# Kernel optimization log

Measured on AMD Instinct MI355X. Metric: run time of the kernel, lower is better.

Reference implementation:

```python
import jax, jax.numpy as jnp
import numpy as np

D_MODEL = 2048
N_HEADS = 16
N_KV = 4
HEAD_DIM = 128
SUB = 64
WINDOW = 512
THETA = 10000.0
NEG = jnp.float32(-1e30)


def _rope_tables(seq_len):
    inv_freq = 1.0 / (THETA ** (jnp.arange(0, HEAD_DIM, 2, dtype=jnp.float32) / HEAD_DIM))
    freqs = jnp.arange(seq_len, dtype=jnp.float32)[:, None] * inv_freq[None, :]  # [S, hd/2]
    emb = jnp.concatenate([freqs, freqs], axis=-1)  # [S, hd]
    return jnp.cos(emb), jnp.sin(emb)


def _rotate_half(x):
    x1, x2 = x[..., : HEAD_DIM // 2], x[..., HEAD_DIM // 2 :]
    return jnp.concatenate([-x2, x1], axis=-1)


def _apply_rope(t, cos, sin):
    # t: [B, H, S, hd]; cos/sin: [S, hd]
    c = cos[None, None]
    s = sin[None, None]
    return t * c + _rotate_half(t) * s


def setup_inputs() -> dict:
    key = jax.random.key(0)
    ks = jax.random.split(key, 6)
    B, S = 1, 2048
    std = 0.02
    return {
        "x": jax.random.normal(ks[0], (B, S, D_MODEL), dtype=jnp.float32),
        "Wq": jax.random.normal(ks[1], (D_MODEL, N_HEADS * HEAD_DIM), dtype=jnp.float32) * std,
        "Wk": jax.random.normal(ks[2], (D_MODEL, N_KV * HEAD_DIM), dtype=jnp.float32) * std,
        "Wv": jax.random.normal(ks[3], (D_MODEL, N_KV * HEAD_DIM), dtype=jnp.float32) * std,
        "Wo": jax.random.normal(ks[4], (N_HEADS * HEAD_DIM, D_MODEL), dtype=jnp.float32) * std,
        "lam": jnp.full((N_HEADS,), 0.1, dtype=jnp.float32),
    }


def reference(x, Wq, Wk, Wv, Wo, lam):
    B, S, _ = x.shape
    n_rep = N_HEADS // N_KV

    q = (x @ Wq).reshape(B, S, N_HEADS, HEAD_DIM).transpose(0, 2, 1, 3)  # [B,H,S,hd]
    k = (x @ Wk).reshape(B, S, N_KV, HEAD_DIM).transpose(0, 2, 1, 3)    # [B,KH,S,hd]
    v = (x @ Wv).reshape(B, S, N_KV, HEAD_DIM).transpose(0, 2, 1, 3)

    cos, sin = _rope_tables(S)
    q = _apply_rope(q, cos, sin)
    k = _apply_rope(k, cos, sin)

    # GQA repeat: each kv head replicated n_rep times consecutively
    k = jnp.repeat(k, n_rep, axis=1)  # [B,H,S,hd]
    v = jnp.repeat(v, n_rep, axis=1)

    q1, q2 = q[..., :SUB], q[..., SUB:]
    k1, k2 = k[..., :SUB], k[..., SUB:]
    scale = 1.0 / jnp.sqrt(jnp.float32(SUB))

    s1 = jnp.einsum("bhqd,bhkd->bhqk", q1, k1) * scale
    s2 = jnp.einsum("bhqd,bhkd->bhqk", q2, k2) * scale

    i = jnp.arange(S)[:, None]
    j = jnp.arange(S)[None, :]
    allowed = (j <= i) & (j >= i - WINDOW + 1)  # causal + sliding window
    s1 = jnp.where(allowed[None, None], s1, NEG)
    s2 = jnp.where(allowed[None, None], s2, NEG)

    a1 = jax.nn.softmax(s1.astype(jnp.float32), axis=-1).astype(x.dtype)
    a2 = jax.nn.softmax(s2.astype(jnp.float32), axis=-1).astype(x.dtype)

    diff = jax.nn.relu(a1 - lam[None, :, None, None] * a2)
    diff = diff / (jnp.sum(diff, axis=-1, keepdims=True) + 1e-6)

    out = jnp.einsum("bhqk,bhkd->bhqd", diff, v)  # [B,H,S,hd]
    out = out.transpose(0, 2, 1, 3).reshape(B, S, N_HEADS * HEAD_DIM)
    return out @ Wo
```

## Files before the change

### kernel.cpp

```cpp
#include <hip/hip_runtime.h>
#include <hip/hip_bf16.h>
#include <stdint.h>

typedef __attribute__((ext_vector_type(8))) short short8;
typedef __attribute__((ext_vector_type(4))) float f32x4;
using bf16 = __hip_bfloat16;

#define MFMA16(a, b, c) __builtin_amdgcn_mfma_f32_16x16x32_bf16((a), (b), (c), 0, 0, 0)

#define GLOAD_LDS16(g, l) __builtin_amdgcn_global_load_lds( \
    (const __attribute__((address_space(1))) void*)(g),     \
    (__attribute__((address_space(3))) void*)(l), 16, 0, 0)

__device__ __forceinline__ unsigned packbf2(float lo, float hi) {
  unsigned r;
  asm("v_cvt_pk_bf16_f32 %0, %1, %2" : "=v"(r) : "v"(lo), "v"(hi));
  return r;
}
__device__ __forceinline__ float ex2(float x) {
  float r;
  asm("v_exp_f32 %0, %1" : "=v"(r) : "v"(x));
  return r;
}
__device__ __forceinline__ f32x4 vmax4(f32x4 a, f32x4 b) {
  f32x4 r;
  r[0] = fmaxf(a[0], b[0]); r[1] = fmaxf(a[1], b[1]);
  r[2] = fmaxf(a[2], b[2]); r[3] = fmaxf(a[3], b[3]);
  return r;
}

template <bool EDGE>
__device__ __forceinline__ void p1_update(const f32x4* sv, float& m, float& l,
                                          int kb0, int myq, int lhi) {
  f32x4 t4 = vmax4(vmax4(sv[0], sv[1]), vmax4(sv[2], sv[3]));
  float tm = fmaxf(fmaxf(t4[0], t4[1]), fmaxf(t4[2], t4[3]));
  float nm = fmaxf(m, tm);
  float sc = ex2(m - nm);
  float sum = 0.f;
#pragma unroll
  for (int nt = 0; nt < 4; ++nt) {
    float part = 0.f;
#pragma unroll
    for (int r = 0; r < 4; ++r) {
      float e = ex2(sv[nt][r] - nm);
      if (EDGE) {
        int key = kb0 + nt * 16 + lhi * 4 + r;
        bool ok = (key <= myq) && (key > myq - 512);
        e = ok ? e : 0.f;
      }
      part += e;
    }
    sum += part;
  }
  l = l * sc + sum;
  m = nm;
}

template <bool EDGE>
__device__ __forceinline__ float p2_probs(const f32x4* s1v, const f32x4* s2v,
                                          float m1, float m2, float c2,
                                          int kb0, int myq, int lhi, int l15,
                                          unsigned* pw) {
  float d0 = 0.f, d1 = 0.f;
#pragma unroll
  for (int nt = 0; nt < 4; ++nt) {
    float pr[4];
#pragma unroll
    for (int r = 0; r < 4; ++r) {
      float e1 = ex2(s1v[nt][r] - m1);
      float e2 = ex2(s2v[nt][r] - m2);
      float p = fmaf(-c2, e2, e1);
      p = fmaxf(p, 0.f);
      if (EDGE) {
        int key = kb0 + nt * 16 + lhi * 4 + r;
        bool ok = (key <= myq) && (key > myq - 512);
        p = ok ? p : 0.f;
      }
      pr[r] = p;
      if (r & 1) d1 += p; else d0 += p;
    }
    int pi = l15 * 36 + 8 * nt + 2 * lhi;
    pw[pi]     = packbf2(pr[0], pr[1]);
    pw[pi + 1] = packbf2(pr[2], pr[3]);
  }
  return d0 + d1;
}

__global__ __launch_bounds__(256) void prep_all(const float* __restrict__ x,
                                                const float* __restrict__ Wq,
                                                const float* __restrict__ Wk,
                                                const float* __restrict__ Wv,
                                                const float* __restrict__ Wo,
                                                bf16* __restrict__ xb,
                                                bf16* __restrict__ WqkvFT,
                                                bf16* __restrict__ WoFT)
{
  const int bx = blockIdx.x;
  const int tid = threadIdx.x;
  if (bx >= 80) {
    size_t i = ((size_t)(bx - 80) * 32 + blockIdx.y) * 2048 + tid * 8;
    const float* f = x + i;
    float4 a = *(const float4*)f;
    float4 b = *(const float4*)(f + 4);
    union { bf16 h[8]; short8 s; } u;
    u.h[0] = __float2bfloat16(a.x); u.h[1] = __float2bfloat16(a.y);
    u.h[2] = __float2bfloat16(a.z); u.h[3] = __float2bfloat16(a.w);
    u.h[4] = __float2bfloat16(b.x); u.h[5] = __float2bfloat16(b.y);
    u.h[6] = __float2bfloat16(b.z); u.h[7] = __float2bfloat16(b.w);
    *(short8*)(xb + i) = u.s;
    return;
  }
  const float* W;
  bf16* Wt;
  int N, n0;
  if (bx < 32)      { W = Wq; Wt = WqkvFT; N = 2048; n0 = bx * 64; }
  else if (bx < 40) { W = Wk; Wt = WqkvFT; N = 512;  n0 = 2048 + (bx - 32) * 64; }
  else if (bx < 48) { W = Wv; Wt = WqkvFT; N = 512;  n0 = 2560 + (bx - 40) * 64; }
  else              { W = Wo; Wt = WoFT;   N = 2048; n0 = (bx - 48) * 64; }
  const int nloc0 = (N == 512) ? (n0 - ((n0 >= 2560) ? 2560 : 2048)) : ((bx < 32 || bx >= 48) ? (n0 & 2047) : 0);
  const int k0 = blockIdx.y * 64;

  __shared__ bf16 t[64][72];
#pragma unroll
  for (int pass = 0; pass < 4; ++pass) {
    int r = pass * 16 + (tid >> 4);
    int c = (tid & 15) * 4;
    float4 v = *(const float4*)(W + (size_t)(k0 + r) * N + nloc0 + c);
    t[c + 0][r] = __float2bfloat16(v.x);
    t[c + 1][r] = __float2bfloat16(v.y);
    t[c + 2][r] = __float2bfloat16(v.z);
    t[c + 3][r] = __float2bfloat16(v.w);
  }
  __syncthreads();
#pragma unroll
  for (int pass = 0; pass < 2; ++pass) {
    int n = pass * 32 + (tid >> 3);
    int k8 = (tid & 7) * 8;
    int frag = ((n0 + n) >> 4) * 64 + ((k0 + k8) >> 5);
    int ln = (n & 15) + 16 * ((k8 >> 3) & 3);
    *(short8*)(Wt + (size_t)frag * 512 + ln * 8) = *(const short8*)(&t[n][k8]);
  }
}

template <int EPI>
__global__ __launch_bounds__(256) void gemm_ft(const bf16* __restrict__ A,
                                               const bf16* __restrict__ Bft,
                                               void* __restrict__ C,
                                               bf16* __restrict__ VTp,
                                               int M, int N, int K)
{
  __shared__ __align__(16) bf16 As[4][128 * 32];

  const int tid  = threadIdx.x;
  const int lane = tid & 63;
  const int w    = tid >> 6;
  const int wmg  = (w >> 1) * 4;
  const int wng  = (w & 1) * 4;
  const int l15  = lane & 15;
  const int lhi  = lane >> 4;

  const int nbx = gridDim.x;
  const int lb  = blockIdx.y * nbx + blockIdx.x;
  const int nwg = nbx * gridDim.y;
  const int lsw = (lb & 7) * (nwg >> 3) + (lb >> 3);
  const int bm0 = (lsw / nbx) * 128;
  const int bn0 = (lsw % nbx) * 128;

  const int srow = lane >> 2;
  const int scol = ((lane & 3) ^ ((lane >> 3) & 3)) * 8;
  const int loff = l15 * 4 + (lhi ^ ((l15 >> 1) & 3));

  const int nkc = K >> 5;
  const bf16* bbase[4];
#pragma unroll
  for (int nt = 0; nt < 4; ++nt)
    bbase[nt] = Bft + ((size_t)((bn0 >> 4) + wng + nt) * nkc) * 512 + lane * 8;

  f32x4 acc[4][4];
  const f32x4 zero4 = {0.f, 0.f, 0.f, 0.f};
#pragma unroll
  for (int i = 0; i < 4; ++i)
#pragma unroll
    for (int j = 0; j < 4; ++j) acc[i][j] = zero4;

  short8 br0[4], br1[4], br2[4], br3[4];

#define GSTAGE_A(buf, kk)                                                          \
  { _Pragma("unroll")                                                              \
    for (int p = 0; p < 2; ++p) {                                                  \
      int s   = (p * 4 + w) * 64 + lane;                                           \
      int row = (p * 4 + w) * 16 + srow;                                           \
      GLOAD_LDS16(A + (size_t)(bm0 + row) * K + (kk) + scol, &As[buf][s * 8]);     \
    } }

#define BLOAD(breg, kc)                                                            \
  { _Pragma("unroll")                                                              \
    for (int nt = 0; nt < 4; ++nt) {                                               \
      asm volatile("global_load_dwordx4 %0, %1, off"                               \
                   : "=v"(breg[nt])                                                \
                   : "v"(bbase[nt] + (size_t)(kc) * 512)                           \
                   : "memory");                                                    \
    } }

#define KSTEP(aslot, breg, wcn, ...)                                               \
  {                                                                                \
    asm volatile("s_waitcnt vmcnt(" #wcn ")" ::: "memory");                        \
    __builtin_amdgcn_s_barrier();                                                  \
    __builtin_amdgcn_sched_barrier(0);                                             \
    __VA_ARGS__                                                                    \
    short8 a_[4];                                                                  \
    _Pragma("unroll")                                                              \
    for (int mt = 0; mt < 4; ++mt)                                                 \
      a_[mt] = *(const short8*)(&As[aslot][((wmg + mt) * 64 + loff) * 8]);         \
    _Pragma("unroll")                                                              \
    for (int mt = 0; mt < 4; ++mt)                                                 \
      _Pragma("unroll")                                                            \
      for (int nt = 0; nt < 4; ++nt)                                               \
        acc[mt][nt] = MFMA16(a_[mt], breg[nt], acc[mt][nt]);                       \
  }

  GSTAGE_A(0, 0);  BLOAD(br0, 0);
  GSTAGE_A(1, 32); BLOAD(br1, 1);
  GSTAGE_A(2, 64); BLOAD(br2, 2);

  for (int t = 0; t < nkc - 4; t += 4) {
    KSTEP(0, br0, 12, GSTAGE_A(3, (t + 3) * 32); BLOAD(br3, t + 3);)
    KSTEP(1, br1, 12, GSTAGE_A(0, (t + 4) * 32); BLOAD(br0, t + 4);)
    KSTEP(2, br2, 12, GSTAGE_A(1, (t + 5) * 32); BLOAD(br1, t + 5);)
    KSTEP(3, br3, 12, GSTAGE_A(2, (t + 6) * 32); BLOAD(br2, t + 6);)
  }
  KSTEP(0, br0, 12, GSTAGE_A(3, (nkc - 1) * 32); BLOAD(br3, nkc - 1);)
  KSTEP(1, br1, 12, )
  KSTEP(2, br2, 6, )
  KSTEP(3, br3, 0, )
#undef GSTAGE_A
#undef BLOAD
#undef KSTEP

  if (EPI == 1) {
#pragma unroll
    for (int mt = 0; mt < 4; ++mt) {
      int row0 = bm0 + (wmg + mt) * 16 + lhi * 4;
#pragma unroll
      for (int nt = 0; nt < 4; ++nt) {
        int col = bn0 + (wng + nt) * 16 + l15;
#pragma unroll
        for (int r = 0; r < 4; ++r)
          ((float*)C)[(size_t)(row0 + r) * N + col] = acc[mt][nt][r];
      }
    }
    return;
  }

  __syncthreads();
  if (bn0 < 2560) {
    float* Lf = (float*)&As[0][0];
    const float scale = (bn0 < 2048) ? 0.180336880111120f : 1.0f;
#pragma unroll
    for (int c = 0; c < 2; ++c) {
      if ((w >> 1) == c) {
#pragma unroll
        for (int mt = 0; mt < 4; ++mt)
#pragma unroll
          for (int nt = 0; nt < 4; ++nt) {
            int col = (wng + nt) * 16 + l15;
#pragma unroll
            for (int r = 0; r < 4; ++r)
              Lf[(mt * 16 + lhi * 4 + r) * 128 + col] = acc[mt][nt][r];
          }
      }
      __syncthreads();
      {
        int rloc = tid >> 2;
        int dg = (tid & 3) * 16;
        int s = bm0 + c * 64 + rloc;
        bf16* orow = (bf16*)C + (size_t)s * N + bn0;
        union { bf16 h[16]; short8 v[2]; } o1, o2;
#pragma unroll
        for (int e = 0; e < 16; ++e) {
          int d = dg + e;
          float inv = __expf(-(float)d * (9.210340371976184f / 64.0f));
          float ang = (float)s * inv;
          float cs = __cosf(ang), sn = __sinf(ang);
          float x1 = Lf[rloc * 128 + d];
          float x2 = Lf[rloc * 128 + d + 64];
          o1.h[e] = __float2bfloat16((x1 * cs - x2 * sn) * scale);
          o2.h[e] = __float2bfloat16((x2 * cs + x1 * sn) * scale);
        }
        *(short8*)(orow + dg)      = o1.v[0];
        *(short8*)(orow + dg + 8)  = o1.v[1];
        *(short8*)(orow + dg + 64) = o2.v[0];
        *(short8*)(orow + dg + 72) = o2.v[1];
      }
      __syncthreads();
    }
  } else {
    bf16* Lb = &As[0][0];
#pragma unroll
    for (int cc = 0; cc < 2; ++cc) {
      if ((w & 1) == cc) {
#pragma unroll
        for (int mt = 0; mt < 4; ++mt)
#pragma unroll
          for (int nt = 0; nt < 4; ++nt) {
            int colloc = nt * 16 + l15;
#pragma unroll
            for (int r = 0; r < 4; ++r) {
              int key = (wmg + mt) * 16 + lhi * 4 + r;
              Lb[colloc * 136 + key] = __float2bfloat16(acc[mt][nt][r]);
            }
          }
      }
      __syncthreads();
      {
        int dl = tid >> 2;
        int kq = (tid & 3) * 32;
        int dim = (bn0 - 2560) + cc * 64 + dl;
        bf16* vrow = VTp + (size_t)dim * 2048 + bm0 + kq;
#pragma unroll
        for (int j = 0; j < 4; ++j)
          *(short8*)(vrow + j * 8) = *(const short8*)(&Lb[dl * 136 + kq + j * 8]);
      }
      __syncthreads();
    }
  }
}

__global__ __launch_bounds__(256) void diff_attn(const bf16* __restrict__ QKV,
                                                 const bf16* __restrict__ VT,
                                                 const float* __restrict__ lam,
                                                 bf16* __restrict__ O)
{
  __shared__ __align__(16) bf16 Kb[2][64 * 128];
  __shared__ __align__(16) bf16 Vb[2][128 * 64];
  __shared__ __align__(16) bf16 Pw[4][16 * 72];

  const int lb  = blockIdx.y * 32 + blockIdx.x;
  const int lsw = (lb & 7) * 64 + (lb >> 3);
  const int qb  = lsw & 31;
  const int h   = lsw >> 5;

  const int kvh  = h >> 2;
  const int tid  = threadIdx.x;
  const int lane = tid & 63;
  const int w    = tid >> 6;
  const int l15  = lane & 15;
  const int lhi  = lane >> 4;
  const int qg   = qb * 64 + w * 16;
  const int myq  = qg + l15;
  const float lamv = lam[h];

  const bf16* Kg = QKV + 2048 + (size_t)kvh * 128;
  const bf16* Vg = VT + (size_t)kvh * 128 * 2048;

  short8 qf[4];
  {
    const bf16* qrow = QKV + (size_t)myq * 3072 + h * 128;
#pragma unroll
    for (int c = 0; c < 4; ++c)
      qf[c] = *(const short8*)(qrow + c * 32 + lhi * 8);
  }

  const int t0 = (qb >= 8) ? (qb - 8) : 0;

#define STAGE_K(buf, kbase)                                                     \
  {                                                                             \
    _Pragma("unroll")                                                           \
    for (int p = 0; p < 4; ++p) {                                               \
      int c = p * 256 + tid;                                                    \
      int r = c >> 4, q = c & 15;                                               \
      GLOAD_LDS16(Kg + (size_t)((kbase) + r) * 3072 + ((q ^ (r & 7)) * 8),      \
                  &Kb[buf][c * 8]);                                             \
    }                                                                           \
  }
#define STAGE_V(buf, kbase)                                                     \
  {                                                                             \
    _Pragma("unroll")                                                           \
    for (int p = 0; p < 4; ++p) {                                               \
      int c = p * 256 + tid;                                                    \
      int d = c >> 3, q = c & 7;                                                \
      GLOAD_LDS16(Vg + (size_t)d * 2048 + (kbase) + ((q ^ (d & 7)) * 8),        \
                  &Vb[buf][c * 8]);                                             \
    }                                                                           \
  }
#define KFRAG(buf, nt, qc) \
  (*(const short8*)(&Kb[buf][(((nt) * 16 + l15) * 16 + ((qc) ^ (((nt) * 16 + l15) & 7))) * 8]))
#define VFRAG(buf, n, qc) \
  (*(const short8*)(&Vb[buf][(((n) * 16 + l15) * 8 + ((qc) ^ (((n) * 16 + l15) & 7))) * 8]))
#define QK_TILE(cur)                                            \
  _Pragma("unroll")                                             \
  for (int nt = 0; nt < 4; ++nt) {                              \
    f32x4 s1 = zero4, s2 = zero4;                               \
    s1 = MFMA16(KFRAG(cur, nt, lhi),      qf[0], s1);           \
    s1 = MFMA16(KFRAG(cur, nt, 4 + lhi),  qf[1], s1);           \
    s2 = MFMA16(KFRAG(cur, nt, 8 + lhi),  qf[2], s2);           \
    s2 = MFMA16(KFRAG(cur, nt, 12 + lhi), qf[3], s2);           \
    s1v[nt] = s1; s2v[nt] = s2;                                 \
  }

  const f32x4 zero4 = {0.f, 0.f, 0.f, 0.f};

  float m1 = -1e30f, l1 = 0.f, m2 = -1e30f, l2 = 0.f;
  STAGE_K(0, t0 * 64);
  asm volatile("s_waitcnt vmcnt(0)" ::: "memory");
  __builtin_amdgcn_s_barrier();
  {
    int cur = 0;
    for (int t = t0; t <= qb; ++t, cur ^= 1) {
      if (t < qb) {
        STAGE_K(cur ^ 1, (t + 1) * 64);
        asm volatile("s_waitcnt vmcnt(4)" ::: "memory");
      } else {
        asm volatile("s_waitcnt vmcnt(0)" ::: "memory");
      }
      __builtin_amdgcn_s_barrier();
      __builtin_amdgcn_sched_barrier(0);
      const int kb0 = t * 64;
      f32x4 s1v[4], s2v[4];
      QK_TILE(cur);
      const bool edge = (t == qb) || (qb >= 8 && t == t0);
      if (edge) {
        p1_update<true>(s1v, m1, l1, kb0, myq, lhi);
        p1_update<true>(s2v, m2, l2, kb0, myq, lhi);
      } else {
        p1_update<false>(s1v, m1, l1, kb0, myq, lhi);
        p1_update<false>(s2v, m2, l2, kb0, myq, lhi);
      }
      __builtin_amdgcn_s_barrier();
    }
  }

#pragma unroll
  for (int mk = 16; mk <= 32; mk <<= 1) {
    float pm = __shfl_xor(m1, mk, 64), pl = __shfl_xor(l1, mk, 64);
    float M = fmaxf(m1, pm);
    l1 = l1 * ex2(m1 - M) + pl * ex2(pm - M);
    m1 = M;
    pm = __shfl_xor(m2, mk, 64); pl = __shfl_xor(l2, mk, 64);
    M = fmaxf(m2, pm);
    l2 = l2 * ex2(m2 - M) + pl * ex2(pm - M);
    m2 = M;
  }
  const float c2 = lamv * l1 / l2;

  f32x4 accv[8];
#pragma unroll
  for (int n = 0; n < 8; ++n) accv[n] = zero4;
  float dln = 0.f;

  STAGE_K(0, t0 * 64);
  STAGE_V(0, t0 * 64);
  asm volatile("s_waitcnt vmcnt(0)" ::: "memory");
  __builtin_amdgcn_s_barrier();
  {
    int cur = 0;
    for (int t = t0; t <= qb; ++t, cur ^= 1) {
      if (t < qb) {
        STAGE_K(cur ^ 1, (t + 1) * 64);
        STAGE_V(cur ^ 1, (t + 1) * 64);
        asm volatile("s_waitcnt vmcnt(8)" ::: "memory");
      } else {
        asm volatile("s_waitcnt vmcnt(0)" ::: "memory");
      }
      __builtin_amdgcn_s_barrier();
      __builtin_amdgcn_sched_barrier(0);
      const int kb0 = t * 64;
      unsigned* pw = (unsigned*)&Pw[w][0];
      f32x4 s1v[4], s2v[4];
      QK_TILE(cur);
      const bool edge = (t == qb) || (qb >= 8 && t == t0);
      if (edge) dln += p2_probs<true>(s1v, s2v, m1, m2, c2, kb0, myq, lhi, l15, pw);
      else      dln += p2_probs<false>(s1v, s2v, m1, m2, c2, kb0, myq, lhi, l15, pw);
#pragma unroll
      for (int kc = 0; kc < 2; ++kc) {
        short8 pa = *(const short8*)(&Pw[w][l15 * 72 + kc * 32 + lhi * 8]);
#pragma unroll
        for (int n = 0; n < 8; ++n)
          accv[n] = MFMA16(pa, VFRAG(cur, n, kc * 4 + lhi), accv[n]);
      }
      __builtin_amdgcn_s_barrier();
    }
  }

  dln += __shfl_xor(dln, 16, 64);
  dln += __shfl_xor(dln, 32, 64);

#pragma unroll
  for (int r = 0; r < 4; ++r) {
    int srcq = lhi * 4 + r;
    int src = (lane & 48) | srcq;
    float dq = __shfl(dln, src, 64);
    float lq = __shfl(l1, src, 64);
    float rinv = 1.f / (dq + lq * 1e-6f);
    int qo = qg + srcq;
#pragma unroll
    for (int n = 0; n < 8; ++n) {
      O[(size_t)qo * 2048 + h * 128 + n * 16 + l15] =
          __float2bfloat16(accv[n][r] * rinv);
    }
  }
#undef STAGE_K
#undef STAGE_V
#undef KFRAG
#undef VFRAG
#undef QK_TILE
}

extern "C" void kernel_launch(void* const* d_in, const int* in_sizes, int n_in,
                              void* d_out, int out_size, void* d_ws, size_t ws_size,
                              hipStream_t stream)
{
  const float* x   = (const float*)d_in[0];
  const float* Wq  = (const float*)d_in[1];
  const float* Wk  = (const float*)d_in[2];
  const float* Wv  = (const float*)d_in[3];
  const float* Wo  = (const float*)d_in[4];
  const float* lam = (const float*)d_in[5];

  char* ws = (char*)d_ws;
  bf16* xb     = (bf16*)(ws);
  bf16* WqkvFT = (bf16*)(ws + 8ull  * (1u << 20));
  bf16* WoFT   = (bf16*)(ws + 20ull * (1u << 20));
  bf16* QKV    = (bf16*)(ws + 28ull * (1u << 20));
  bf16* ATT    = (bf16*)(ws + 40ull * (1u << 20));
  bf16* VT     = (bf16*)(ws + 48ull * (1u << 20));

  prep_all<<<dim3(144, 32), 256, 0, stream>>>(x, Wq, Wk, Wv, Wo, xb, WqkvFT, WoFT);
  gemm_ft<0><<<dim3(24, 16), 256, 0, stream>>>(xb, WqkvFT, QKV, VT, 2048, 3072, 2048);
  diff_attn<<<dim3(32, 16), 256, 0, stream>>>(QKV, VT, lam, ATT);
  gemm_ft<1><<<dim3(16, 16), 256, 0, stream>>>(ATT, WoFT, d_out, nullptr, 2048, 2048, 2048);
}
```

Before: 110.9 us.

## Split QKV GEMM into dedicated 128x256-tile 512-thread kernel with direct V-transpose stores

The QKV projection gets its own kernel with 8 waves and a 128x256 output tile. This halves the grid to 192 workgroups and lets each A tile in LDS be reused across twice as many output columns. The V epilogue now packs accumulators and writes the transposed layout straight to global memory, with no LDS staging or extra barriers. The output-projection GEMM is split into its own plain fp32-store kernel. Risks are fewer workgroups than CUs (192 on a 256-CU part), higher register pressure, and scattered 8-byte stores for the V transpose.

```diff
diff --git a/kernel.cpp b/kernel.cpp
--- a/kernel.cpp
+++ b/kernel.cpp
@@ -142,11 +142,162 @@
   }
 }
 
-template <int EPI>
-__global__ __launch_bounds__(256) void gemm_ft(const bf16* __restrict__ A,
+__global__ __launch_bounds__(512) void gemm_qkv(const bf16* __restrict__ A,
+                                                const bf16* __restrict__ Bft,
+                                                bf16* __restrict__ QKV,
+                                                bf16* __restrict__ VTp,
+                                                int M, int N, int K)
+{
+  __shared__ __align__(16) char smem[65536];
+  bf16* As = (bf16*)smem;
+
+  const int tid  = threadIdx.x;
+  const int lane = tid & 63;
+  const int w    = tid >> 6;
+  const int wmg  = (w >> 2) * 4;
+  const int wng  = (w & 3) * 4;
+  const int l15  = lane & 15;
+  const int lhi  = lane >> 4;
+
+  const int nbx = gridDim.x;
+  const int lb  = blockIdx.y * nbx + blockIdx.x;
+  const int nwg = nbx * gridDim.y;
+  const int lsw = (lb & 7) * (nwg >> 3) + (lb >> 3);
+  const int bm0 = (lsw / nbx) * 128;
+  const int bn0 = (lsw % nbx) * 256;
+
+  const int srow = tid >> 2;
+  const int scol = ((tid & 3) ^ ((tid >> 3) & 3)) * 8;
+  const int loff = l15 * 4 + (lhi ^ ((l15 >> 1) & 3));
+
+  const int nkc = K >> 5;
+  const bf16* bbase[4];
+#pragma unroll
+  for (int nt = 0; nt < 4; ++nt)
+    bbase[nt] = Bft + ((size_t)((bn0 >> 4) + wng + nt) * nkc) * 512 + lane * 8;
+
+  f32x4 acc[4][4];
+  const f32x4 zero4 = {0.f, 0.f, 0.f, 0.f};
+#pragma unroll
+  for (int i = 0; i < 4; ++i)
+#pragma unroll
+    for (int j = 0; j < 4; ++j) acc[i][j] = zero4;
+
+  short8 br0[4], br1[4], br2[4], br3[4];
+
+#define GSTAGE_A(buf, kk)                                                           \
+  { GLOAD_LDS16(A + (size_t)(bm0 + srow) * K + (kk) + scol,                         \
+                As + (buf) * 4096 + tid * 8); }
+
+#define BLOAD(breg, kc)                                                             \
+  { _Pragma("unroll")                                                               \
+    for (int nt = 0; nt < 4; ++nt) {                                                \
+      asm volatile("global_load_dwordx4 %0, %1, off"                                \
+                   : "=v"(breg[nt])                                                 \
+                   : "v"(bbase[nt] + (size_t)(kc) * 512)                            \
+                   : "memory");                                                     \
+    } }
+
+#define KSTEP(aslot, breg, wcn, ...)                                                \
+  {                                                                                 \
+    asm volatile("s_waitcnt vmcnt(" #wcn ")" ::: "memory");                         \
+    __builtin_amdgcn_s_barrier();                                                   \
+    __builtin_amdgcn_sched_barrier(0);                                              \
+    __VA_ARGS__                                                                     \
+    short8 a_[4];                                                                   \
+    _Pragma("unroll")                                                               \
+    for (int mt = 0; mt < 4; ++mt)                                                  \
+      a_[mt] = *(const short8*)(As + (aslot) * 4096 + ((wmg + mt) * 64 + loff) * 8);\
+    _Pragma("unroll")                                                               \
+    for (int mt = 0; mt < 4; ++mt)                                                  \
+      _Pragma("unroll")                                                             \
+      for (int nt = 0; nt < 4; ++nt)                                                \
+        acc[mt][nt] = MFMA16(a_[mt], breg[nt], acc[mt][nt]);                        \
+  }
+
+  GSTAGE_A(0, 0);  BLOAD(br0, 0);
+  GSTAGE_A(1, 32); BLOAD(br1, 1);
+  GSTAGE_A(2, 64); BLOAD(br2, 2);
+
+  for (int t = 0; t < nkc - 4; t += 4) {
+    KSTEP(0, br0, 10, GSTAGE_A(3, (t + 3) * 32); BLOAD(br3, t + 3);)
+    KSTEP(1, br1, 10, GSTAGE_A(0, (t + 4) * 32); BLOAD(br0, t + 4);)
+    KSTEP(2, br2, 10, GSTAGE_A(1, (t + 5) * 32); BLOAD(br1, t + 5);)
+    KSTEP(3, br3, 10, GSTAGE_A(2, (t + 6) * 32); BLOAD(br2, t + 6);)
+  }
+  KSTEP(0, br0, 10, GSTAGE_A(3, (nkc - 1) * 32); BLOAD(br3, nkc - 1);)
+  KSTEP(1, br1, 10, )
+  KSTEP(2, br2, 5, )
+  KSTEP(3, br3, 0, )
+#undef GSTAGE_A
+#undef BLOAD
+#undef KSTEP
+
+  __syncthreads();
+  if (bn0 < 2560) {
+    float* Lf = (float*)smem;
+    const float scale = (bn0 < 2048) ? 0.180336880111120f : 1.0f;
+#pragma unroll
+    for (int half = 0; half < 2; ++half) {
+      if ((w >> 2) == half) {
+#pragma unroll
+        for (int mt = 0; mt < 4; ++mt)
+#pragma unroll
+          for (int nt = 0; nt < 4; ++nt) {
+            int col = (w & 3) * 64 + nt * 16 + l15;
+#pragma unroll
+            for (int r = 0; r < 4; ++r)
+              Lf[(mt * 16 + lhi * 4 + r) * 256 + col] = acc[mt][nt][r];
+          }
+      }
+      __syncthreads();
+      {
+        int row = tid >> 3;
+        int pg = (tid & 7) * 16;
+        int head = pg >> 6;
+        int din0 = pg & 63;
+        int col1 = head * 128 + din0;
+        int s = bm0 + half * 64 + row;
+        bf16* orow = QKV + (size_t)s * 3072 + bn0;
+        union { bf16 h[16]; short8 v[2]; } o1, o2;
+#pragma unroll
+        for (int e = 0; e < 16; ++e) {
+          int din = din0 + e;
+          float inv = __expf(-(float)din * (9.210340371976184f / 64.0f));
+          float ang = (float)s * inv;
+          float cs = __cosf(ang), sn = __sinf(ang);
+          float x1 = Lf[row * 256 + col1 + e];
+          float x2 = Lf[row * 256 + col1 + e + 64];
+          o1.h[e] = __float2bfloat16((x1 * cs - x2 * sn) * scale);
+          o2.h[e] = __float2bfloat16((x2 * cs + x1 * sn) * scale);
+        }
+        *(short8*)(orow + col1)      = o1.v[0];
+        *(short8*)(orow + col1 + 8)  = o1.v[1];
+        *(short8*)(orow + col1 + 64) = o2.v[0];
+        *(short8*)(orow + col1 + 72) = o2.v[1];
+      }
+      __syncthreads();
+    }
+  } else {
+    const int dimbase = (bn0 - 2560) + (w & 3) * 64;
+#pragma unroll
+    for (int mt = 0; mt < 4; ++mt) {
+#pragma unroll
+      for (int nt = 0; nt < 4; ++nt) {
+        int dim = dimbase + nt * 16 + l15;
+        int key0 = bm0 + (w >> 2) * 64 + mt * 16 + lhi * 4;
+        uint2 pk;
+        pk.x = packbf2(acc[mt][nt][0], acc[mt][nt][1]);
+        pk.y = packbf2(acc[mt][nt][2], acc[mt][nt][3]);
+        *(uint2*)(VTp + (size_t)dim * 2048 + key0) = pk;
+      }
+    }
+  }
+}
+
+__global__ __launch_bounds__(256) void gemm_wo(const bf16* __restrict__ A,
                                                const bf16* __restrict__ Bft,
-                                               void* __restrict__ C,
-                                               bf16* __restrict__ VTp,
+                                               float* __restrict__ C,
                                                int M, int N, int K)
 {
   __shared__ __align__(16) bf16 As[4][128 * 32];
@@ -237,91 +388,15 @@
 #undef BLOAD
 #undef KSTEP
 
-  if (EPI == 1) {
-#pragma unroll
-    for (int mt = 0; mt < 4; ++mt) {
-      int row0 = bm0 + (wmg + mt) * 16 + lhi * 4;
-#pragma unroll
-      for (int nt = 0; nt < 4; ++nt) {
-        int col = bn0 + (wng + nt) * 16 + l15;
-#pragma unroll
-        for (int r = 0; r < 4; ++r)
-          ((float*)C)[(size_t)(row0 + r) * N + col] = acc[mt][nt][r];
-      }
-    }
-    return;
-  }
-
-  __syncthreads();
-  if (bn0 < 2560) {
-    float* Lf = (float*)&As[0][0];
-    const float scale = (bn0 < 2048) ? 0.180336880111120f : 1.0f;
-#pragma unroll
-    for (int c = 0; c < 2; ++c) {
-      if ((w >> 1) == c) {
-#pragma unroll
-        for (int mt = 0; mt < 4; ++mt)
-#pragma unroll
-          for (int nt = 0; nt < 4; ++nt) {
-            int col = (wng + nt) * 16 + l15;
-#pragma unroll
-            for (int r = 0; r < 4; ++r)
-              Lf[(mt * 16 + lhi * 4 + r) * 128 + col] = acc[mt][nt][r];
-          }
-      }
-      __syncthreads();
-      {
-        int rloc = tid >> 2;
-        int dg = (tid & 3) * 16;
-        int s = bm0 + c * 64 + rloc;
-        bf16* orow = (bf16*)C + (size_t)s * N + bn0;
-        union { bf16 h[16]; short8 v[2]; } o1, o2;
-#pragma unroll
-        for (int e = 0; e < 16; ++e) {
-          int d = dg + e;
-          float inv = __expf(-(float)d * (9.210340371976184f / 64.0f));
-          float ang = (float)s * inv;
-          float cs = __cosf(ang), sn = __sinf(ang);
-          float x1 = Lf[rloc * 128 + d];
-          float x2 = Lf[rloc * 128 + d + 64];
-          o1.h[e] = __float2bfloat16((x1 * cs - x2 * sn) * scale);
-          o2.h[e] = __float2bfloat16((x2 * cs + x1 * sn) * scale);
-        }
-        *(short8*)(orow + dg)      = o1.v[0];
-        *(short8*)(orow + dg + 8)  = o1.v[1];
-        *(short8*)(orow + dg + 64) = o2.v[0];
-        *(short8*)(orow + dg + 72) = o2.v[1];
-      }
-      __syncthreads();
-    }
-  } else {
-    bf16* Lb = &As[0][0];
-#pragma unroll
-    for (int cc = 0; cc < 2; ++cc) {
-      if ((w & 1) == cc) {
-#pragma unroll
-        for (int mt = 0; mt < 4; ++mt)
-#pragma unroll
-          for (int nt = 0; nt < 4; ++nt) {
-            int colloc = nt * 16 + l15;
-#pragma unroll
-            for (int r = 0; r < 4; ++r) {
-              int key = (wmg + mt) * 16 + lhi * 4 + r;
-              Lb[colloc * 136 + key] = __float2bfloat16(acc[mt][nt][r]);
-            }
-          }
-      }
-      __syncthreads();
-      {
-        int dl = tid >> 2;
-        int kq = (tid & 3) * 32;
-        int dim = (bn0 - 2560) + cc * 64 + dl;
-        bf16* vrow = VTp + (size_t)dim * 2048 + bm0 + kq;
-#pragma unroll
-        for (int j = 0; j < 4; ++j)
-          *(short8*)(vrow + j * 8) = *(const short8*)(&Lb[dl * 136 + kq + j * 8]);
-      }
-      __syncthreads();
+#pragma unroll
+  for (int mt = 0; mt < 4; ++mt) {
+    int row0 = bm0 + (wmg + mt) * 16 + lhi * 4;
+#pragma unroll
+    for (int nt = 0; nt < 4; ++nt) {
+      int col = bn0 + (wng + nt) * 16 + l15;
+#pragma unroll
+      for (int r = 0; r < 4; ++r)
+        C[(size_t)(row0 + r) * N + col] = acc[mt][nt][r];
     }
   }
 }
@@ -526,7 +601,7 @@
   bf16* VT     = (bf16*)(ws + 48ull * (1u << 20));
 
   prep_all<<<dim3(144, 32), 256, 0, stream>>>(x, Wq, Wk, Wv, Wo, xb, WqkvFT, WoFT);
-  gemm_ft<0><<<dim3(24, 16), 256, 0, stream>>>(xb, WqkvFT, QKV, VT, 2048, 3072, 2048);
+  gemm_qkv<<<dim3(12, 16), 512, 0, stream>>>(xb, WqkvFT, QKV, VT, 2048, 3072, 2048);
   diff_attn<<<dim3(32, 16), 256, 0, stream>>>(QKV, VT, lam, ATT);
-  gemm_ft<1><<<dim3(16, 16), 256, 0, stream>>>(ATT, WoFT, d_out, nullptr, 2048, 2048, 2048);
-}
+  gemm_wo<<<dim3(16, 16), 256, 0, stream>>>(ATT, WoFT, (float*)d_out, 2048, 2048, 2048);
+}
```

After: 106.6 us. 3.9% less time.
